# Kernel tuning notes

Hardware: AMD Instinct MI355X
Metric: run time of the kernel (lower is better)

## Reference

```python
import jax, jax.numpy as jnp
import numpy as np

DIM = 1024
HEAD_DIM = 64
CHUNK = 128
B, T = 4, 4096


def setup_inputs() -> dict:
    key = jax.random.key(0)
    ks = jax.random.split(key, 8)
    s = 1.0 / np.sqrt(DIM)
    inp = {
        'x': jax.random.normal(ks[0], (B, T, DIM), jnp.float32),
        'Wq': jax.random.normal(ks[1], (DIM, DIM), jnp.float32) * s,
        'bq': jnp.zeros((DIM,), jnp.float32),
        'Wk': jax.random.normal(ks[2], (DIM, DIM), jnp.float32) * s,
        'bk': jnp.zeros((DIM,), jnp.float32),
        'Wv': jax.random.normal(ks[3], (DIM, DIM), jnp.float32) * s,
        'bv': jnp.zeros((DIM,), jnp.float32),
        'Wbeta': jax.random.normal(ks[4], (DIM, DIM), jnp.float32) * s,
        'bbeta': jnp.zeros((DIM,), jnp.float32),
        'Walpha': jax.random.normal(ks[5], (DIM, DIM), jnp.float32) * s,
        'balpha': jnp.full((DIM,), 2.0, jnp.float32),  # bias init 2.0 as in torch
    }
    return inp


def reference(x, Wq, bq, Wk, bk, Wv, bv, Wbeta, bbeta, Walpha, balpha):
    Bsz, Tlen, D = x.shape
    d = HEAD_DIM
    H = D // d
    C = CHUNK
    scale = d ** (-0.5)

    q = ((x @ Wq.T + bq) * scale).reshape(Bsz, Tlen, H, d)
    k = ((x @ Wk.T + bk) * scale).reshape(Bsz, Tlen, H, d)
    v = (x @ Wv.T + bv).reshape(Bsz, Tlen, H, d)
    alpha_logits = jnp.clip((x @ Walpha.T + balpha).reshape(Bsz, Tlen, H, d), -10.0, 10.0)
    log_alpha = jax.nn.log_sigmoid(alpha_logits)
    alpha_val = jax.nn.sigmoid(alpha_logits)
    beta = jax.nn.softplus(x @ Wbeta.T + bbeta).reshape(Bsz, Tlen, H, d)

    # pad T to a multiple of C (static)
    pad = (-Tlen) % C
    if pad:
        pw = ((0, 0), (0, pad), (0, 0), (0, 0))
        q, k, v = jnp.pad(q, pw), jnp.pad(k, pw), jnp.pad(v, pw)
        log_alpha, beta = jnp.pad(log_alpha, pw), jnp.pad(beta, pw)
    N = q.shape[1] // C
    cshape = (Bsz, N, C, H, d)
    q, k, v = q.reshape(cshape), k.reshape(cshape), v.reshape(cshape)
    log_alpha, beta = log_alpha.reshape(cshape), beta.reshape(cshape)

    ccum = jnp.cumsum(log_alpha, axis=2)          # (B,N,C,H,d)
    m = ccum.mean(axis=-1)                        # (B,N,C,H); mean is linear -> take before pairwise diff
    decay_logits_mean = m[:, :, :, None, :] - m[:, :, None, :, :]  # (B,N,C,C,H)
    tril = jnp.tril(jnp.ones((C, C), jnp.float32))[None, None, :, :, None]
    decay_logits_mean = jnp.where(tril == 0, -1e9, decay_logits_mean)
    decay = jnp.exp(decay_logits_mean)            # (B,N,C,C,H)

    attn = jnp.einsum('bnihd,bnjhd->bnhij', q, k)
    attn = attn * decay.transpose(0, 1, 4, 2, 3)
    y_intra = jnp.einsum('bnhij,bnjhd->bnihd', attn, v * beta)  # (B,N,C,H,d)

    # inter-chunk recurrence via scan over chunks
    asum = jnp.exp(log_alpha.sum(axis=2).mean(axis=-1))  # (B,N,H) total chunk decay
    curve = jnp.exp(m)                                   # (B,N,C,H) intra-chunk decay curve
    bmean = beta.mean(axis=-1)                           # (B,N,C,H)

    def to_scan(a):
        return jnp.moveaxis(a, 1, 0)
    xs = (to_scan(q), to_scan(y_intra), to_scan(curve), to_scan(asum),
          to_scan(k), to_scan(v), to_scan(bmean))

    state0 = jnp.zeros((Bsz, H, d, d), jnp.float32)

    def step(state, inputs):
        qi, yi, ci, ai, ki, vi, bmi = inputs
        mem = jnp.einsum('bchq,bhqk->bchk', qi, state)
        y = yi + mem * ci[..., None]
        state = state * ai[:, :, None, None]
        delta = jnp.einsum('bchk,bchv,bch->bhkv', ki, vi, bmi)
        return state + delta, y

    state, ys = jax.lax.scan(step, state0, xs)
    y = jnp.moveaxis(ys, 0, 1).reshape(Bsz, N * C, D)
    if pad:
        y = y[:, :Tlen, :]
    return y, state, alpha_val
```

## Files before the change

### kernel.cpp

```cpp
#include <hip/hip_runtime.h>
#include <cstdint>
#include <cmath>

#define DIMM 1024
#define NHEAD 16
#define HEADD 64
#define CHUNKC 128
#define NBATCH 4
#define TLEN 4096
#define NCHUNK 32
#define BT (NBATCH * TLEN)
#define NSTACK (5 * DIMM)

typedef unsigned short ushort_t;
typedef __attribute__((ext_vector_type(8))) short short8;
typedef __attribute__((ext_vector_type(4))) float f32x4;

__device__ __forceinline__ float blo(unsigned int u) { return __uint_as_float(u << 16); }
__device__ __forceinline__ float bhi(unsigned int u) { return __uint_as_float(u & 0xffff0000u); }
__device__ __forceinline__ ushort_t f2bf(float f) {
  unsigned int u = __float_as_uint(f);
  u += 0x7fffu + ((u >> 16) & 1u);
  return (ushort_t)(u >> 16);
}
__device__ __forceinline__ float bf2f(ushort_t s) { return __uint_as_float(((unsigned int)s) << 16); }
__device__ __forceinline__ unsigned pack2(float a, float b) {
  return (unsigned)f2bf(a) | ((unsigned)f2bf(b) << 16);
}

__device__ __forceinline__ void async16(const ushort_t* g, ushort_t* l) {
  __builtin_amdgcn_global_load_lds((__attribute__((address_space(1))) void*)g,
                                   (__attribute__((address_space(3))) void*)l, 16, 0, 0);
}

__global__ __launch_bounds__(256) void k_cast(
    const float* __restrict__ x,
    const float* __restrict__ Wq, const float* __restrict__ Wk,
    const float* __restrict__ Wv, const float* __restrict__ Wb, const float* __restrict__ Wa,
    const float* __restrict__ bq, const float* __restrict__ bk,
    const float* __restrict__ bv, const float* __restrict__ bb, const float* __restrict__ ba,
    ushort_t* __restrict__ xb, ushort_t* __restrict__ wbm, float* __restrict__ bias_st) {
  const long XU = (long)BT * DIMM / 4;
  const long WU = (long)NSTACK * DIMM / 4;
  const long BU = NSTACK / 4;
  const long NU = XU + WU + BU;
  for (long u = (long)blockIdx.x * blockDim.x + threadIdx.x; u < NU;
       u += (long)gridDim.x * blockDim.x) {
    if (u < XU) {
      float4 f = ((const float4*)x)[u];
      ushort4 o;
      o.x = f2bf(f.x); o.y = f2bf(f.y); o.z = f2bf(f.z); o.w = f2bf(f.w);
      ((ushort4*)xb)[u] = o;
    } else if (u < XU + WU) {
      long j = u - XU;
      long e = j * 4;
      int row = (int)(e >> 10);
      int col = (int)(e & 1023);
      int p = row >> 10, wr = row & 1023;
      const float* Wp = (p == 0) ? Wq : (p == 1) ? Wk : (p == 2) ? Wv : (p == 3) ? Wb : Wa;
      float4 f = *(const float4*)(Wp + (size_t)wr * DIMM + col);
      ushort4 o;
      o.x = f2bf(f.x); o.y = f2bf(f.y); o.z = f2bf(f.z); o.w = f2bf(f.w);
      ((ushort4*)wbm)[j] = o;
    } else {
      long j = u - XU - WU;
      int e = (int)(j * 4);
      int p = e >> 10, r = e & 1023;
      const float* bp = (p == 0) ? bq : (p == 1) ? bk : (p == 2) ? bv : (p == 3) ? bb : ba;
      ((float4*)bias_st)[j] = *(const float4*)(bp + r);
    }
  }
}

__global__ __launch_bounds__(256) void k_proj(
    const ushort_t* __restrict__ xb, const ushort_t* __restrict__ wbm,
    const float* __restrict__ bias_st,
    ushort_t* __restrict__ qo, ushort_t* __restrict__ ko,
    ushort_t* __restrict__ vo, ushort_t* __restrict__ bo,
    float* __restrict__ ao) {
  __shared__ ushort_t As[128 * 32];
  __shared__ ushort_t Bs[128 * 32];
  const int tid = threadIdx.x;
  const int bn0 = blockIdx.x * 128;
  const int bm0 = blockIdx.y * 128;
  const int lane = tid & 63;
  const int wave = tid >> 6;
  const int quad = lane >> 4, lr = lane & 15;
  const int wr = (wave >> 1) * 64, wc = (wave & 1) * 64;

  f32x4 zero = {0.f, 0.f, 0.f, 0.f};
  f32x4 acc[4][4];
#pragma unroll
  for (int i = 0; i < 4; ++i)
#pragma unroll
    for (int j = 0; j < 4; ++j) acc[i][j] = zero;

  const int r0 = tid >> 2;
  const int c0 = (tid & 3) * 8;
  const ushort_t* ag0 = xb + (size_t)(bm0 + r0) * DIMM + c0;
  const ushort_t* ag1 = xb + (size_t)(bm0 + r0 + 64) * DIMM + c0;
  const ushort_t* bg0 = wbm + (size_t)(bn0 + r0) * DIMM + c0;
  const ushort_t* bg1 = wbm + (size_t)(bn0 + r0 + 64) * DIMM + c0;
  ushort_t* la0 = As + tid * 8;
  ushort_t* la1 = As + 2048 + tid * 8;
  ushort_t* lb0 = Bs + tid * 8;
  ushort_t* lb1 = Bs + 2048 + tid * 8;

  for (int kk = 0; kk < DIMM; kk += 32) {
    __syncthreads();
    async16(ag0 + kk, la0);
    async16(ag1 + kk, la1);
    async16(bg0 + kk, lb0);
    async16(bg1 + kk, lb1);
    __syncthreads();
    short8 af[4], bfr[4];
#pragma unroll
    for (int i = 0; i < 4; ++i)
      af[i] = *(const short8*)(As + (wr + i * 16 + lr) * 32 + quad * 8);
#pragma unroll
    for (int j = 0; j < 4; ++j)
      bfr[j] = *(const short8*)(Bs + (wc + j * 16 + lr) * 32 + quad * 8);
#pragma unroll
    for (int i = 0; i < 4; ++i)
#pragma unroll
      for (int j = 0; j < 4; ++j)
        acc[i][j] = __builtin_amdgcn_mfma_f32_16x16x32_bf16(af[i], bfr[j], acc[i][j], 0, 0, 0);
  }

  const int p = bn0 >> 10;
  const int ncol0 = bn0 & 1023;
#pragma unroll
  for (int j = 0; j < 4; ++j) {
    const int colg = wc + j * 16 + lr;
    const float bias = bias_st[bn0 + colg];
    const int nc = ncol0 + colg;
#pragma unroll
    for (int i = 0; i < 4; ++i) {
#pragma unroll
      for (int r = 0; r < 4; ++r) {
        const int rowl = wr + i * 16 + quad * 4 + r;
        const size_t o = (size_t)(bm0 + rowl) * DIMM + nc;
        float val = acc[i][j][r] + bias;
        if (p == 0) {
          qo[o] = f2bf(val * 0.125f);
        } else if (p == 1) {
          ko[o] = f2bf(val * 0.125f);
        } else if (p == 2) {
          vo[o] = f2bf(val);
        } else if (p == 3) {
          float sp = (val > 20.f) ? val : log1pf(expf(val));
          bo[o] = f2bf(sp);
        } else {
          float c = fminf(fmaxf(val, -10.f), 10.f);
          ao[o] = 1.f / (1.f + expf(-c));
        }
      }
    }
  }
}

__global__ __launch_bounds__(128) void k_stats(
    const float* __restrict__ alpha, const ushort_t* __restrict__ betaw,
    float* __restrict__ mArr, float* __restrict__ bmean, float* __restrict__ asum) {
  const int bnh = blockIdx.x;
  const int h = bnh & 15, n = (bnh >> 4) & 31, b = bnh >> 9;
  const int c = threadIdx.x;
  const size_t bt = (size_t)b * TLEN + n * CHUNKC + c;

  const float4* ap = (const float4*)(alpha + bt * DIMM + h * HEADD);
  float ls = 0.f;
#pragma unroll
  for (int w = 0; w < 16; ++w) {
    float4 a = ap[w];
    ls += logf(a.x) + logf(a.y) + logf(a.z) + logf(a.w);
  }
  const uint4* bp = (const uint4*)(betaw + bt * DIMM + h * HEADD);
  float bs = 0.f;
#pragma unroll
  for (int w = 0; w < 8; ++w) {
    uint4 u = bp[w];
    bs += blo(u.x) + bhi(u.x) + blo(u.y) + bhi(u.y) + blo(u.z) + bhi(u.z) + blo(u.w) + bhi(u.w);
  }
  float la = ls * (1.f / 64.f);

  __shared__ float s[128];
  s[c] = la;
  __syncthreads();
  for (int off = 1; off < 128; off <<= 1) {
    float t = (c >= off) ? s[c - off] : 0.f;
    __syncthreads();
    s[c] += t;
    __syncthreads();
  }
  float m = s[c];
  const size_t o = (size_t)bnh * CHUNKC + c;
  mArr[o] = m;
  bmean[o] = bs * (1.f / 64.f);
  if (c == 127) asum[bnh] = expf(m);
}

__global__ __launch_bounds__(256) void k_delta(
    const ushort_t* __restrict__ kw, const ushort_t* __restrict__ vw,
    const float* __restrict__ bmean, float* __restrict__ delta) {
  __shared__ ushort_t kc[8192];
  __shared__ ushort_t vc[8192];
  __shared__ float bm[128];
  const int bnh = blockIdx.x;
  const int h = bnh & 15, n = (bnh >> 4) & 31, b = bnh >> 9;
  const int tid = threadIdx.x;
  const size_t bt0 = (size_t)b * TLEN + n * CHUNKC;

#pragma unroll
  for (int it = 0; it < 4; ++it) {
    int u = tid + it * 256;
    int row = u >> 3, col = (u & 7) * 8;
    size_t go = (bt0 + row) * DIMM + h * HEADD + col;
    ((uint4*)kc)[u] = *(const uint4*)(kw + go);
    ((uint4*)vc)[u] = *(const uint4*)(vw + go);
  }
  if (tid < 128) bm[tid] = bmean[(size_t)bnh * CHUNKC + tid];
  __syncthreads();

  const int kd = tid >> 2, v0 = (tid & 3) * 16;
  float acc[16];
#pragma unroll
  for (int l = 0; l < 16; ++l) acc[l] = 0.f;

#pragma unroll 4
  for (int c = 0; c < 128; ++c) {
    float kb = bf2f(kc[c * 64 + kd]) * bm[c];
    const uint4* vr = (const uint4*)(vc + c * 64 + v0);
    uint4 u0 = vr[0], u1 = vr[1];
    acc[0] += kb * blo(u0.x);  acc[1] += kb * bhi(u0.x);
    acc[2] += kb * blo(u0.y);  acc[3] += kb * bhi(u0.y);
    acc[4] += kb * blo(u0.z);  acc[5] += kb * bhi(u0.z);
    acc[6] += kb * blo(u0.w);  acc[7] += kb * bhi(u0.w);
    acc[8] += kb * blo(u1.x);  acc[9] += kb * bhi(u1.x);
    acc[10] += kb * blo(u1.y); acc[11] += kb * bhi(u1.y);
    acc[12] += kb * blo(u1.z); acc[13] += kb * bhi(u1.z);
    acc[14] += kb * blo(u1.w); acc[15] += kb * bhi(u1.w);
  }
  float* dst = delta + (size_t)bnh * 4096 + kd * 64 + v0;
#pragma unroll
  for (int l4 = 0; l4 < 4; ++l4)
    ((float4*)dst)[l4] = make_float4(acc[l4 * 4], acc[l4 * 4 + 1], acc[l4 * 4 + 2], acc[l4 * 4 + 3]);
}

__global__ __launch_bounds__(256) void k_scan(
    const float* __restrict__ delta, const float* __restrict__ asum,
    float* __restrict__ Earr, float* __restrict__ state_out) {
  const int bh = blockIdx.x >> 4;
  const int g = blockIdx.x & 15;
  const int b = bh >> 4, h = bh & 15;
  const int elem = g * 256 + threadIdx.x;
  float e = 0.f;
  for (int n = 0; n < 32; ++n) {
    const size_t o = (((size_t)b * 32 + n) * 16 + h) * 4096 + elem;
    const float a = asum[((size_t)b * 32 + n) * 16 + h];
    Earr[o] = e;
    e = e * a + delta[o];
  }
  state_out[(size_t)bh * 4096 + elem] = e;
}

__global__ __launch_bounds__(256) void k_y(
    const ushort_t* __restrict__ qw, const ushort_t* __restrict__ kw,
    const ushort_t* __restrict__ vw, const ushort_t* __restrict__ betaw,
    const float* __restrict__ mArr, const float* __restrict__ Earr,
    float* __restrict__ yout) {
  __shared__ __align__(16) ushort_t vbt[64][200];
  __shared__ __align__(16) ushort_t pst[4][32][40];
  __shared__ float ms[128];
  const int bnh = blockIdx.x;
  const int h = bnh & 15, n = (bnh >> 4) & 31, b = bnh >> 9;
  const int tid = threadIdx.x;
  const int lane = tid & 63;
  const int wv = tid >> 6;
  const int quad = lane >> 4, lr = lane & 15;
  const int i0 = wv * 32;
  const size_t bt0 = (size_t)b * TLEN + n * CHUNKC;
  const size_t hoff = (size_t)h * HEADD;

#pragma unroll
  for (int it = 0; it < 4; ++it) {
    int u = tid + it * 256;
    int j = u & 127, vd0 = (u >> 7) * 8;
    size_t go = (bt0 + j) * DIMM + hoff + vd0;
    uint4 vv = *(const uint4*)(vw + go);
    uint4 bb2 = *(const uint4*)(betaw + go);
    vbt[vd0 + 0][j] = f2bf(blo(vv.x) * blo(bb2.x));
    vbt[vd0 + 1][j] = f2bf(bhi(vv.x) * bhi(bb2.x));
    vbt[vd0 + 2][j] = f2bf(blo(vv.y) * blo(bb2.y));
    vbt[vd0 + 3][j] = f2bf(bhi(vv.y) * bhi(bb2.y));
    vbt[vd0 + 4][j] = f2bf(blo(vv.z) * blo(bb2.z));
    vbt[vd0 + 5][j] = f2bf(bhi(vv.z) * bhi(bb2.z));
    vbt[vd0 + 6][j] = f2bf(blo(vv.w) * blo(bb2.w));
    vbt[vd0 + 7][j] = f2bf(bhi(vv.w) * bhi(bb2.w));
  }
  const float4* Eg = (const float4*)(Earr + (size_t)bnh * 4096);
#pragma unroll
  for (int it = 0; it < 4; ++it) {
    int u = tid + it * 256;
    int kd = u >> 4, vd0 = (u & 15) * 4;
    float4 ev = Eg[u];
    vbt[vd0 + 0][128 + kd] = f2bf(ev.x);
    vbt[vd0 + 1][128 + kd] = f2bf(ev.y);
    vbt[vd0 + 2][128 + kd] = f2bf(ev.z);
    vbt[vd0 + 3][128 + kd] = f2bf(ev.w);
  }
  if (tid < 128) ms[tid] = mArr[(size_t)bnh * CHUNKC + tid];
  __syncthreads();

  short8 qa[2][2];
#pragma unroll
  for (int it = 0; it < 2; ++it) {
    const ushort_t* qg = qw + (bt0 + i0 + it * 16 + lr) * DIMM + hoff + quad * 8;
    qa[it][0] = *(const short8*)(qg);
    qa[it][1] = *(const short8*)(qg + 32);
  }
  float mi[2][4];
#pragma unroll
  for (int it = 0; it < 2; ++it)
#pragma unroll
    for (int r = 0; r < 4; ++r) mi[it][r] = ms[i0 + it * 16 + quad * 4 + r];

  f32x4 zero = {0.f, 0.f, 0.f, 0.f};
  f32x4 acc2[2][4];
#pragma unroll
  for (int it = 0; it < 2; ++it)
#pragma unroll
    for (int nt = 0; nt < 4; ++nt) acc2[it][nt] = zero;

  for (int js = 0; js < 4; ++js) {
    const int j0 = js * 32;
#pragma unroll
    for (int jsub = 0; jsub < 2; ++jsub) {
      const int j0s = j0 + jsub * 16;
      const ushort_t* kg = kw + (bt0 + j0s + lr) * DIMM + hoff + quad * 8;
      short8 kb0 = *(const short8*)(kg);
      short8 kb1 = *(const short8*)(kg + 32);
      const float mj = ms[j0s + lr];
#pragma unroll
      for (int it = 0; it < 2; ++it) {
        f32x4 s = __builtin_amdgcn_mfma_f32_16x16x32_bf16(qa[it][0], kb0, zero, 0, 0, 0);
        s = __builtin_amdgcn_mfma_f32_16x16x32_bf16(qa[it][1], kb1, s, 0, 0, 0);
#pragma unroll
        for (int r = 0; r < 4; ++r) {
          const int ig = i0 + it * 16 + quad * 4 + r;
          const int jg = j0s + lr;
          float w = (jg > ig) ? 0.f : s[r] * __expf(mi[it][r] - mj);
          pst[wv][it * 16 + quad * 4 + r][jsub * 16 + lr] = f2bf(w);
        }
      }
    }
#pragma unroll
    for (int it = 0; it < 2; ++it) {
      short8 pa = *(const short8*)&pst[wv][it * 16 + lr][quad * 8];
#pragma unroll
      for (int nt = 0; nt < 4; ++nt) {
        short8 vb = *(const short8*)&vbt[nt * 16 + lr][j0 + quad * 8];
        acc2[it][nt] = __builtin_amdgcn_mfma_f32_16x16x32_bf16(pa, vb, acc2[it][nt], 0, 0, 0);
      }
    }
  }

#pragma unroll
  for (int es = 0; es < 2; ++es) {
    const int kd0 = es * 32;
    {
      const int row = lane >> 1;
      const int col0 = (lane & 1) * 16;
      const float ex = __expf(ms[i0 + row]);
      const ushort_t* qg = qw + (bt0 + i0 + row) * DIMM + hoff + kd0 + col0;
      uint4 u0 = *(const uint4*)(qg);
      uint4 u1 = *(const uint4*)(qg + 8);
      uint4 w0, w1;
      w0.x = pack2(blo(u0.x) * ex, bhi(u0.x) * ex);
      w0.y = pack2(blo(u0.y) * ex, bhi(u0.y) * ex);
      w0.z = pack2(blo(u0.z) * ex, bhi(u0.z) * ex);
      w0.w = pack2(blo(u0.w) * ex, bhi(u0.w) * ex);
      w1.x = pack2(blo(u1.x) * ex, bhi(u1.x) * ex);
      w1.y = pack2(blo(u1.y) * ex, bhi(u1.y) * ex);
      w1.z = pack2(blo(u1.z) * ex, bhi(u1.z) * ex);
      w1.w = pack2(blo(u1.w) * ex, bhi(u1.w) * ex);
      *(uint4*)&pst[wv][row][col0] = w0;
      *(uint4*)&pst[wv][row][col0 + 8] = w1;
    }
#pragma unroll
    for (int it = 0; it < 2; ++it) {
      short8 pa = *(const short8*)&pst[wv][it * 16 + lr][quad * 8];
#pragma unroll
      for (int nt = 0; nt < 4; ++nt) {
        short8 vb = *(const short8*)&vbt[nt * 16 + lr][128 + kd0 + quad * 8];
        acc2[it][nt] = __builtin_amdgcn_mfma_f32_16x16x32_bf16(pa, vb, acc2[it][nt], 0, 0, 0);
      }
    }
  }

#pragma unroll
  for (int it = 0; it < 2; ++it) {
#pragma unroll
    for (int nt = 0; nt < 4; ++nt) {
      f32x4 a = acc2[it][nt];
#pragma unroll
      for (int r = 0; r < 4; ++r) {
        const int ig = i0 + it * 16 + quad * 4 + r;
        yout[(bt0 + ig) * DIMM + hoff + nt * 16 + lr] = a[r];
      }
    }
  }
}

extern "C" void kernel_launch(void* const* d_in, const int* in_sizes, int n_in,
                              void* d_out, int out_size, void* d_ws, size_t ws_size,
                              hipStream_t stream) {
  const float* x  = (const float*)d_in[0];
  const float* Wq = (const float*)d_in[1];
  const float* bq = (const float*)d_in[2];
  const float* Wk = (const float*)d_in[3];
  const float* bk = (const float*)d_in[4];
  const float* Wv = (const float*)d_in[5];
  const float* bv = (const float*)d_in[6];
  const float* Wb = (const float*)d_in[7];
  const float* bb = (const float*)d_in[8];
  const float* Wa = (const float*)d_in[9];
  const float* ba = (const float*)d_in[10];

  char* ws = (char*)d_ws;
  ushort_t* xb   = (ushort_t*)(ws + 0);
  ushort_t* wbm  = (ushort_t*)(ws + 33554432);
  float* bias_st = (float*)(ws + 44040192);
  ushort_t* qw   = (ushort_t*)(ws + 44060672);
  ushort_t* kw   = (ushort_t*)(ws + 77615104);
  ushort_t* vw   = (ushort_t*)(ws + 111169536);
  ushort_t* bw   = (ushort_t*)(ws + 144723968);
  float* mArr    = (float*)(ws + 178278400);
  float* bmean   = (float*)(ws + 179326976);
  float* asum    = (float*)(ws + 180375552);
  float* delta   = (float*)(ws + 180383744);
  float* Earr    = (float*)(ws + 213938176);

  float* yout = (float*)d_out;
  float* state_out = yout + (size_t)BT * DIMM;
  float* aout = state_out + (size_t)NBATCH * NHEAD * 64 * 64;

  k_cast<<<dim3(4096), dim3(256), 0, stream>>>(x, Wq, Wk, Wv, Wb, Wa,
                                               bq, bk, bv, bb, ba, xb, wbm, bias_st);
  k_proj<<<dim3(40, 128), dim3(256), 0, stream>>>(xb, wbm, bias_st, qw, kw, vw, bw, aout);
  k_stats<<<dim3(2048), dim3(128), 0, stream>>>(aout, bw, mArr, bmean, asum);
  k_delta<<<dim3(2048), dim3(256), 0, stream>>>(kw, vw, bmean, delta);
  k_scan<<<dim3(1024), dim3(256), 0, stream>>>(delta, asum, Earr, state_out);
  k_y<<<dim3(2048), dim3(256), 0, stream>>>(qw, kw, vw, bw, mArr, Earr, yout);
}
```

Measured before the change: 671.7 us.

## Swizzle projection GEMM LDS layout and stage bf16 epilogue through shared memory

Reorders the global-to-LDS load mapping so each MFMA fragment is stored contiguously per lane, which removes the strided LDS reads that caused bank conflicts. For the bf16 outputs (q, k, v, beta), the epilogue now writes results into a padded shared-memory tile in two halves and then emits 16-byte coalesced global stores, replacing scattered 2-byte stores. The alpha float path keeps direct stores. The cost is extra barriers and reuse of LDS in the epilogue.

```diff
diff --git a/kernel.cpp b/kernel.cpp
--- a/kernel.cpp
+++ b/kernel.cpp
@@ -78,15 +78,20 @@
     ushort_t* __restrict__ qo, ushort_t* __restrict__ ko,
     ushort_t* __restrict__ vo, ushort_t* __restrict__ bo,
     float* __restrict__ ao) {
-  __shared__ ushort_t As[128 * 32];
-  __shared__ ushort_t Bs[128 * 32];
+  __shared__ __align__(16) char smem[18432];
+  ushort_t* As = (ushort_t*)smem;
+  ushort_t* Bs = (ushort_t*)(smem + 8192);
+  ushort_t* Cs = (ushort_t*)smem;
+
   const int tid = threadIdx.x;
   const int bn0 = blockIdx.x * 128;
   const int bm0 = blockIdx.y * 128;
   const int lane = tid & 63;
-  const int wave = tid >> 6;
+  const int wv = tid >> 6;
   const int quad = lane >> 4, lr = lane & 15;
-  const int wr = (wave >> 1) * 64, wc = (wave & 1) * 64;
+  const int wr = (wv >> 1) * 64, wc = (wv & 1) * 64;
+  const int g4a = (wv >> 1) * 4;
+  const int g4b = (wv & 1) * 4;
 
   f32x4 zero = {0.f, 0.f, 0.f, 0.f};
   f32x4 acc[4][4];
@@ -95,12 +100,12 @@
 #pragma unroll
     for (int j = 0; j < 4; ++j) acc[i][j] = zero;
 
-  const int r0 = tid >> 2;
-  const int c0 = (tid & 3) * 8;
-  const ushort_t* ag0 = xb + (size_t)(bm0 + r0) * DIMM + c0;
-  const ushort_t* ag1 = xb + (size_t)(bm0 + r0 + 64) * DIMM + c0;
-  const ushort_t* bg0 = wbm + (size_t)(bn0 + r0) * DIMM + c0;
-  const ushort_t* bg1 = wbm + (size_t)(bn0 + r0 + 64) * DIMM + c0;
+  const int rowA = ((tid >> 6) & 3) * 16 + (tid & 15);
+  const int colA = ((tid >> 4) & 3) * 8;
+  const ushort_t* ag0 = xb + (size_t)(bm0 + rowA) * DIMM + colA;
+  const ushort_t* ag1 = xb + (size_t)(bm0 + 64 + rowA) * DIMM + colA;
+  const ushort_t* bg0 = wbm + (size_t)(bn0 + rowA) * DIMM + colA;
+  const ushort_t* bg1 = wbm + (size_t)(bn0 + 64 + rowA) * DIMM + colA;
   ushort_t* la0 = As + tid * 8;
   ushort_t* la1 = As + 2048 + tid * 8;
   ushort_t* lb0 = Bs + tid * 8;
@@ -116,10 +121,10 @@
     short8 af[4], bfr[4];
 #pragma unroll
     for (int i = 0; i < 4; ++i)
-      af[i] = *(const short8*)(As + (wr + i * 16 + lr) * 32 + quad * 8);
+      af[i] = *(const short8*)(As + ((g4a + i) * 64 + lane) * 8);
 #pragma unroll
     for (int j = 0; j < 4; ++j)
-      bfr[j] = *(const short8*)(Bs + (wc + j * 16 + lr) * 32 + quad * 8);
+      bfr[j] = *(const short8*)(Bs + ((g4b + j) * 64 + lane) * 8);
 #pragma unroll
     for (int i = 0; i < 4; ++i)
 #pragma unroll
@@ -129,31 +134,55 @@
 
   const int p = bn0 >> 10;
   const int ncol0 = bn0 & 1023;
-#pragma unroll
-  for (int j = 0; j < 4; ++j) {
-    const int colg = wc + j * 16 + lr;
-    const float bias = bias_st[bn0 + colg];
-    const int nc = ncol0 + colg;
-#pragma unroll
-    for (int i = 0; i < 4; ++i) {
-#pragma unroll
-      for (int r = 0; r < 4; ++r) {
-        const int rowl = wr + i * 16 + quad * 4 + r;
-        const size_t o = (size_t)(bm0 + rowl) * DIMM + nc;
-        float val = acc[i][j][r] + bias;
-        if (p == 0) {
-          qo[o] = f2bf(val * 0.125f);
-        } else if (p == 1) {
-          ko[o] = f2bf(val * 0.125f);
-        } else if (p == 2) {
-          vo[o] = f2bf(val);
-        } else if (p == 3) {
-          float sp = (val > 20.f) ? val : log1pf(expf(val));
-          bo[o] = f2bf(sp);
-        } else {
+
+  if (p == 4) {
+#pragma unroll
+    for (int j = 0; j < 4; ++j) {
+      const int colg = wc + j * 16 + lr;
+      const float bias = bias_st[bn0 + colg];
+      const int nc = ncol0 + colg;
+#pragma unroll
+      for (int i = 0; i < 4; ++i) {
+#pragma unroll
+        for (int r = 0; r < 4; ++r) {
+          const int rowl = wr + i * 16 + quad * 4 + r;
+          float val = acc[i][j][r] + bias;
           float c = fminf(fmaxf(val, -10.f), 10.f);
-          ao[o] = 1.f / (1.f + expf(-c));
+          ao[(size_t)(bm0 + rowl) * DIMM + nc] = 1.f / (1.f + expf(-c));
         }
+      }
+    }
+  } else {
+    ushort_t* outp = (p == 0) ? qo : (p == 1) ? ko : (p == 2) ? vo : bo;
+    const float qs = (p <= 1) ? 0.125f : 1.f;
+    for (int hf = 0; hf < 2; ++hf) {
+      __syncthreads();
+      if ((wv & 1) == hf) {
+#pragma unroll
+        for (int j = 0; j < 4; ++j) {
+          const int colg = wc + j * 16 + lr;
+          const float bias = bias_st[bn0 + colg];
+          const int scol = j * 16 + lr;
+#pragma unroll
+          for (int i = 0; i < 4; ++i) {
+#pragma unroll
+            for (int r = 0; r < 4; ++r) {
+              const int rowl = wr + i * 16 + quad * 4 + r;
+              float val = acc[i][j][r] + bias;
+              if (p == 3) val = (val > 20.f) ? val : log1pf(expf(val));
+              else val *= qs;
+              Cs[rowl * 72 + scol] = f2bf(val);
+            }
+          }
+        }
+      }
+      __syncthreads();
+#pragma unroll
+      for (int it2 = 0; it2 < 4; ++it2) {
+        const int u = tid + it2 * 256;
+        const int row = u >> 3, ch = u & 7;
+        uint4 w = *(const uint4*)(Cs + row * 72 + ch * 8);
+        *(uint4*)(outp + (size_t)(bm0 + row) * DIMM + ncol0 + hf * 64 + ch * 8) = w;
       }
     }
   }
```

New measurement: 782.1 us. +16.4%, slower.
